# Kernel tuning notes

Measured on AMD Instinct MI355X. Metric: run time of the kernel, lower is better.

Reference implementation:

```python
import jax, jax.numpy as jnp
import numpy as np

N = 50000       # nodes
E = 800000      # edges (avg degree 16)
IN_FEATS = 256
HEADS = 8
OUT_FEATS = 32
SLOPE = 0.2     # LeakyReLU negative slope


def setup_inputs() -> dict:
    key = jax.random.key(0)
    k1, k2, k3, k4, k5, k6 = jax.random.split(key, 6)
    feat = jax.random.normal(k1, (N, IN_FEATS), dtype=jnp.float32)
    # xavier-ish scaling for the linear weight, stored [in, out] for jax
    fc_w = jax.random.normal(k2, (IN_FEATS, HEADS * OUT_FEATS), dtype=jnp.float32) / np.sqrt(IN_FEATS)
    attn_l = jax.random.normal(k3, (HEADS, OUT_FEATS), dtype=jnp.float32) * 0.1
    attn_r = jax.random.normal(k4, (HEADS, OUT_FEATS), dtype=jnp.float32) * 0.1
    src = jax.random.randint(k5, (E,), 0, N, dtype=jnp.int32)
    dst = jnp.sort(jax.random.randint(k6, (E,), 0, N, dtype=jnp.int32))
    return {"feat": feat, "fc_w": fc_w, "attn_l": attn_l, "attn_r": attn_r,
            "src": src, "dst": dst}


def reference(feat, fc_w, attn_l, attn_r, src, dst):
    # dense projection: [N, H, F]
    feat_src = (feat @ fc_w).reshape(N, HEADS, OUT_FEATS)
    el = jnp.einsum('nhf,hf->nh', feat_src, attn_l)   # [N, H]
    er = jnp.einsum('nhf,hf->nh', feat_src, attn_r)   # [N, H]

    # per-edge raw score: nb.el + v.er  -> [E, H]
    e = el[src] + er[dst]
    # per-destination max over incoming edges (edge softmax stabilizer)
    m = jax.ops.segment_max(e, dst, num_segments=N)   # [N, H]
    z = e - m[dst]
    # Seastar order: exp(leaky_relu(emb - max(embs)))
    coeff = jnp.exp(jnp.where(z >= 0, z, SLOPE * z))  # [E, H]
    s = jax.ops.segment_sum(coeff, dst, num_segments=N)
    alpha = coeff / s[dst]                            # [E, H]

    # weighted scatter-sum of gathered neighbor features -> [N, H, F]
    out = jax.ops.segment_sum(alpha[:, :, None] * feat_src[src], dst, num_segments=N)
    return out
```

## Files before the change

kernel.cpp:

```cpp
#include <hip/hip_runtime.h>
#include <hip/hip_bf16.h>

#define N_NODES 50000
#define N_EDGES 800000
#define IN_F 256
#define HEADS 8
#define OUT_F 32
#define HF (HEADS * OUT_F)
#define SLOPE 0.2f

typedef __attribute__((ext_vector_type(8))) short bf16x8;
typedef __attribute__((ext_vector_type(4))) float f32x4;

__device__ __forceinline__ ushort f2bf(float f) {
  union { float f; unsigned u; } x;
  x.f = f;
  unsigned r = x.u + 0x7FFFu + ((x.u >> 16) & 1u);
  return (ushort)(r >> 16);
}

__device__ __forceinline__ float bf2f_lo(unsigned u) {
  return __uint_as_float(u << 16);
}
__device__ __forceinline__ float bf2f_hi(unsigned u) {
  return __uint_as_float(u & 0xFFFF0000u);
}

__global__ void wt_kernel(const float* __restrict__ fc_w,
                          ushort* __restrict__ Bt) {
  __shared__ float tile[32][33];
  const int bx = blockIdx.x * 32;
  const int by = blockIdx.y * 32;
  const int tx = threadIdx.x;
  const int ty = threadIdx.y;
#pragma unroll
  for (int i = 0; i < 32; i += 8)
    tile[ty + i][tx] = fc_w[(size_t)(by + ty + i) * HF + bx + tx];
  __syncthreads();
#pragma unroll
  for (int i = 0; i < 32; i += 8)
    Bt[(size_t)(bx + ty + i) * IN_F + by + tx] = f2bf(tile[tx][ty + i]);
}

#define BM 64
#define BN 256
#define BK 32
#define LDA 40

__global__ __launch_bounds__(256) void gemm_mfma(
    const float* __restrict__ A, const ushort* __restrict__ Bt,
    ushort* __restrict__ Cb, int M) {
  __shared__ __align__(16) ushort As[BM * LDA];
  __shared__ __align__(16) ushort Bs[BN * LDA];

  const int t = threadIdx.x;
  const int wave = t >> 6;
  const int lane = t & 63;
  const int m0 = blockIdx.x * BM;

  const int ar = t >> 2;
  const int ak = (t & 3) * 8;
  const int br = t >> 2;
  const int bk = (t & 3) * 8;

  const int q = lane >> 4;
  const int l16 = lane & 15;
  const int wn = wave * 64;

  f32x4 acc[4][4] = {};

  for (int k0 = 0; k0 < IN_F; k0 += BK) {
    {
      float4 v0 = make_float4(0.f, 0.f, 0.f, 0.f);
      float4 v1 = make_float4(0.f, 0.f, 0.f, 0.f);
      if (m0 + ar < M) {
        const float* ap = &A[(size_t)(m0 + ar) * IN_F + k0 + ak];
        v0 = *(const float4*)ap;
        v1 = *(const float4*)(ap + 4);
      }
      union { ushort s[8]; uint4 v; } u;
      u.s[0] = f2bf(v0.x); u.s[1] = f2bf(v0.y);
      u.s[2] = f2bf(v0.z); u.s[3] = f2bf(v0.w);
      u.s[4] = f2bf(v1.x); u.s[5] = f2bf(v1.y);
      u.s[6] = f2bf(v1.z); u.s[7] = f2bf(v1.w);
      *(uint4*)&As[ar * LDA + ak] = u.v;
    }
#pragma unroll
    for (int i = 0; i < 4; ++i) {
      const int n = br + i * 64;
      *(uint4*)&Bs[n * LDA + bk] =
          *(const uint4*)&Bt[(size_t)n * IN_F + k0 + bk];
    }
    __syncthreads();

    bf16x8 aF[4], bF[4];
#pragma unroll
    for (int i = 0; i < 4; ++i)
      aF[i] = *(const bf16x8*)&As[(i * 16 + l16) * LDA + q * 8];
#pragma unroll
    for (int jj = 0; jj < 4; ++jj)
      bF[jj] = *(const bf16x8*)&Bs[(wn + jj * 16 + l16) * LDA + q * 8];
#pragma unroll
    for (int i = 0; i < 4; ++i)
#pragma unroll
      for (int jj = 0; jj < 4; ++jj)
        acc[i][jj] = __builtin_amdgcn_mfma_f32_16x16x32_bf16(
            aF[i], bF[jj], acc[i][jj], 0, 0, 0);
    __syncthreads();
  }

#pragma unroll
  for (int i = 0; i < 4; ++i) {
#pragma unroll
    for (int r = 0; r < 4; ++r) {
      const int row = m0 + 16 * i + q * 4 + r;
      if (row < M) {
#pragma unroll
        for (int jj = 0; jj < 4; ++jj) {
          const int col = wn + 16 * jj + l16;
          Cb[(size_t)row * HF + col] = f2bf(acc[i][jj][r]);
        }
      }
    }
  }
}

__global__ void wl_kernel(const float* __restrict__ fc_w,
                          const float* __restrict__ attn_l,
                          float* __restrict__ wl) {
  const int idx = blockIdx.x * blockDim.x + threadIdx.x;
  const int k = idx >> 3;
  const int h = idx & 7;
  const float* fp = &fc_w[(size_t)k * HF + h * OUT_F];
  const float* ap = &attn_l[h * OUT_F];
  float acc = 0.f;
#pragma unroll
  for (int f = 0; f < OUT_F; f += 4) {
    float4 a = *(const float4*)&fp[f];
    float4 b = *(const float4*)&ap[f];
    acc += a.x * b.x + a.y * b.y + a.z * b.z + a.w * b.w;
  }
  wl[idx] = acc;
}

__global__ __launch_bounds__(256) void el_kernel(
    const float* __restrict__ feat, const float* __restrict__ wl,
    float* __restrict__ el, int NH) {
  __shared__ float wls[IN_F * HEADS];
  const int t = threadIdx.x;
#pragma unroll
  for (int i = 0; i < (IN_F * HEADS) / 256; ++i)
    wls[i * 256 + t] = wl[i * 256 + t];
  __syncthreads();

  const int idx = blockIdx.x * 256 + t;
  if (idx >= NH) return;
  const int n = idx >> 3;
  const int h = idx & 7;
  const float* fp = &feat[(size_t)n * IN_F];
  float acc = 0.f;
#pragma unroll 8
  for (int k0 = 0; k0 < IN_F; k0 += 4) {
    float4 v = *(const float4*)&fp[k0];
    acc += v.x * wls[(k0 + 0) * 8 + h] + v.y * wls[(k0 + 1) * 8 + h] +
           v.z * wls[(k0 + 2) * 8 + h] + v.w * wls[(k0 + 3) * 8 + h];
  }
  el[idx] = acc;
}

__global__ void rowptr_kernel(const int* __restrict__ dst,
                              int* __restrict__ row_ptr, int N, int E) {
  int i = blockIdx.x * blockDim.x + threadIdx.x;
  if (i > N) return;
  int lo = 0, hi = E;
  while (lo < hi) {
    int mid = (lo + hi) >> 1;
    if (dst[mid] < i) lo = mid + 1; else hi = mid;
  }
  row_ptr[i] = lo;
}

#define CHUNK 64

__global__ __launch_bounds__(256) void aggregate_kernel(
    const ushort* __restrict__ featb, const float* __restrict__ el,
    const int* __restrict__ src, const int* __restrict__ row_ptr,
    float* __restrict__ out) {
  const int v = blockIdx.x;
  const int t = threadIdx.x;
  const int beg = row_ptr[v];
  const int deg = row_ptr[v + 1] - beg;

  if (deg == 0) {
    out[(size_t)v * HF + t] = 0.f;
    return;
  }

  __shared__ float s_wred[4][HEADS];
  __shared__ __align__(16) float s_alpha[CHUNK][HEADS];
  __shared__ int s_src[CHUNK];
  __shared__ __align__(16) float s_out[4][HF];

  const int lane = t & 63;
  const int wave = t >> 6;
  const int j = t >> 3;
  const int h8 = t & 7;
  const int h = lane >> 3;

  float mx = -1e30f;
  for (int e = j; e < deg; e += 32)
    mx = fmaxf(mx, el[(size_t)src[beg + e] * HEADS + h8]);
  mx = fmaxf(mx, __shfl_xor(mx, 8));
  mx = fmaxf(mx, __shfl_xor(mx, 16));
  mx = fmaxf(mx, __shfl_xor(mx, 32));
  if (lane < HEADS) s_wred[wave][lane] = mx;
  __syncthreads();
  const float m = fmaxf(fmaxf(s_wred[0][h8], s_wred[1][h8]),
                        fmaxf(s_wred[2][h8], s_wred[3][h8]));

  float4 acc = make_float4(0.f, 0.f, 0.f, 0.f);
  float ssum = 0.f;

  for (int c0 = 0; c0 < deg; c0 += CHUNK) {
    const int cn = min(CHUNK, deg - c0);
    const int cnp = (cn + 3) & ~3;
    __syncthreads();
    for (int cc = j; cc < cnp; cc += 32) {
      if (cc < cn) {
        const int s = src[beg + c0 + cc];
        if (h8 == 0) s_src[cc] = s;
        const float z = el[(size_t)s * HEADS + h8] - m;
        const float w = (z >= 0.f) ? z : SLOPE * z;
        const float cf = __expf(w);
        s_alpha[cc][h8] = cf;
        ssum += cf;
      } else {
        if (h8 == 0) s_src[cc] = 0;
        s_alpha[cc][h8] = 0.f;
      }
    }
    __syncthreads();
#pragma unroll 2
    for (int e0 = 0; e0 < cnp; e0 += 4) {
      const int e = e0 + wave;
      const int s = s_src[e];
      const float a = s_alpha[e][h];
      const uint2 u = *(const uint2*)&featb[(size_t)s * HF + lane * 4];
      acc.x = fmaf(a, bf2f_lo(u.x), acc.x);
      acc.y = fmaf(a, bf2f_hi(u.x), acc.y);
      acc.z = fmaf(a, bf2f_lo(u.y), acc.z);
      acc.w = fmaf(a, bf2f_hi(u.y), acc.w);
    }
  }

  ssum += __shfl_xor(ssum, 8);
  ssum += __shfl_xor(ssum, 16);
  ssum += __shfl_xor(ssum, 32);
  if (lane < HEADS) s_wred[wave][lane] = ssum;
  *(float4*)&s_out[wave][lane * 4] = acc;
  __syncthreads();

  const int ho = t >> 5;
  const float ssum_all =
      s_wred[0][ho] + s_wred[1][ho] + s_wred[2][ho] + s_wred[3][ho];
  const float r = s_out[0][t] + s_out[1][t] + s_out[2][t] + s_out[3][t];
  out[(size_t)v * HF + t] = r / ssum_all;
}

extern "C" void kernel_launch(void* const* d_in, const int* in_sizes, int n_in,
                              void* d_out, int out_size, void* d_ws,
                              size_t ws_size, hipStream_t stream) {
  const float* feat = (const float*)d_in[0];
  const float* fc_w = (const float*)d_in[1];
  const float* attn_l = (const float*)d_in[2];
  const int* src = (const int*)d_in[4];
  const int* dst = (const int*)d_in[5];
  float* out = (float*)d_out;

  const int N = N_NODES;
  const int E = N_EDGES;

  ushort* featb = (ushort*)d_ws;
  float* el = (float*)(featb + (size_t)N * HF);
  float* wl = el + (size_t)N * HEADS;
  ushort* Bt = (ushort*)(wl + IN_F * HEADS);
  int* row_ptr = (int*)(Bt + (size_t)IN_F * HF);

  wt_kernel<<<dim3(8, 8), dim3(32, 8), 0, stream>>>(fc_w, Bt);

  gemm_mfma<<<(N + BM - 1) / BM, 256, 0, stream>>>(feat, Bt, featb, N);

  wl_kernel<<<(IN_F * HEADS) / 256, 256, 0, stream>>>(fc_w, attn_l, wl);

  el_kernel<<<(N * HEADS + 255) / 256, 256, 0, stream>>>(feat, wl, el,
                                                         N * HEADS);

  rowptr_kernel<<<(N + 1 + 255) / 256, 256, 0, stream>>>(dst, row_ptr, N, E);

  aggregate_kernel<<<N, 256, 0, stream>>>(featb, el, src, row_ptr, out);
}
```

Before: 250.0 us.

## Merge prep kernels, transpose wl in LDS, prefetch neighbor features for low-degree nodes

Three small setup kernels (weight transpose, wl projection, row_ptr binary search) become one launch with block-index dispatch, cutting launch overhead. el_kernel stores wl transposed per head in LDS so each thread can read float4 weights instead of strided scalars. For nodes with degree up to 64, aggregate_kernel issues all neighbor feature gathers into registers before the max/softmax phase, so gather latency overlaps with the score computation and one chunk sync is removed. The prefetch uses 16 uint2 registers per thread, which raises register pressure and may lower occupancy.

After: 264.3 us. 1.06x slower.

```diff
diff --git a/kernel.cpp b/kernel.cpp
--- a/kernel.cpp
+++ b/kernel.cpp
@@ -26,20 +26,56 @@
   return __uint_as_float(u & 0xFFFF0000u);
 }
 
-__global__ void wt_kernel(const float* __restrict__ fc_w,
-                          ushort* __restrict__ Bt) {
+#define ROWPTR_BLOCKS ((N_NODES + 1 + 255) / 256)
+
+__global__ __launch_bounds__(256) void prep_kernel(
+    const float* __restrict__ fc_w, const float* __restrict__ attn_l,
+    ushort* __restrict__ Bt, float* __restrict__ wl,
+    const int* __restrict__ dst, int* __restrict__ row_ptr) {
   __shared__ float tile[32][33];
-  const int bx = blockIdx.x * 32;
-  const int by = blockIdx.y * 32;
-  const int tx = threadIdx.x;
-  const int ty = threadIdx.y;
-#pragma unroll
-  for (int i = 0; i < 32; i += 8)
-    tile[ty + i][tx] = fc_w[(size_t)(by + ty + i) * HF + bx + tx];
-  __syncthreads();
-#pragma unroll
-  for (int i = 0; i < 32; i += 8)
-    Bt[(size_t)(bx + ty + i) * IN_F + by + tx] = f2bf(tile[tx][ty + i]);
+  const int b = blockIdx.x;
+  const int t = threadIdx.x;
+
+  if (b < 64) {
+    const int bx = (b & 7) * 32;
+    const int by = (b >> 3) * 32;
+    const int tx = t & 31;
+    const int ty = t >> 5;
+#pragma unroll
+    for (int i = 0; i < 32; i += 8)
+      tile[ty + i][tx] = fc_w[(size_t)(by + ty + i) * HF + bx + tx];
+    __syncthreads();
+#pragma unroll
+    for (int i = 0; i < 32; i += 8)
+      Bt[(size_t)(bx + ty + i) * IN_F + by + tx] = f2bf(tile[tx][ty + i]);
+  } else if (b == 64) {
+#pragma unroll
+    for (int ii = 0; ii < 8; ++ii) {
+      const int idx = ii * 256 + t;
+      const int k = idx >> 3;
+      const int h = idx & 7;
+      const float* fp = &fc_w[(size_t)k * HF + h * OUT_F];
+      const float* ap = &attn_l[h * OUT_F];
+      float acc = 0.f;
+#pragma unroll
+      for (int f = 0; f < OUT_F; f += 4) {
+        float4 a = *(const float4*)&fp[f];
+        float4 bb = *(const float4*)&ap[f];
+        acc += a.x * bb.x + a.y * bb.y + a.z * bb.z + a.w * bb.w;
+      }
+      wl[idx] = acc;
+    }
+  } else {
+    const int i = (b - 65) * 256 + t;
+    if (i <= N_NODES) {
+      int lo = 0, hi = N_EDGES;
+      while (lo < hi) {
+        int mid = (lo + hi) >> 1;
+        if (dst[mid] < i) lo = mid + 1; else hi = mid;
+      }
+      row_ptr[i] = lo;
+    }
+  }
 }
 
 #define BM 64
@@ -125,32 +161,16 @@
   }
 }
 
-__global__ void wl_kernel(const float* __restrict__ fc_w,
-                          const float* __restrict__ attn_l,
-                          float* __restrict__ wl) {
-  const int idx = blockIdx.x * blockDim.x + threadIdx.x;
-  const int k = idx >> 3;
-  const int h = idx & 7;
-  const float* fp = &fc_w[(size_t)k * HF + h * OUT_F];
-  const float* ap = &attn_l[h * OUT_F];
-  float acc = 0.f;
-#pragma unroll
-  for (int f = 0; f < OUT_F; f += 4) {
-    float4 a = *(const float4*)&fp[f];
-    float4 b = *(const float4*)&ap[f];
-    acc += a.x * b.x + a.y * b.y + a.z * b.z + a.w * b.w;
-  }
-  wl[idx] = acc;
-}
-
 __global__ __launch_bounds__(256) void el_kernel(
     const float* __restrict__ feat, const float* __restrict__ wl,
     float* __restrict__ el, int NH) {
-  __shared__ float wls[IN_F * HEADS];
+  __shared__ __align__(16) float wlsT[HEADS][IN_F + 4];
   const int t = threadIdx.x;
 #pragma unroll
-  for (int i = 0; i < (IN_F * HEADS) / 256; ++i)
-    wls[i * 256 + t] = wl[i * 256 + t];
+  for (int i = 0; i < (IN_F * HEADS) / 256; ++i) {
+    const int idx = i * 256 + t;
+    wlsT[idx & 7][idx >> 3] = wl[idx];
+  }
   __syncthreads();
 
   const int idx = blockIdx.x * 256 + t;
@@ -158,29 +178,16 @@
   const int n = idx >> 3;
   const int h = idx & 7;
   const float* fp = &feat[(size_t)n * IN_F];
+  const float* wp = &wlsT[h][0];
   float acc = 0.f;
 #pragma unroll 8
   for (int k0 = 0; k0 < IN_F; k0 += 4) {
     float4 v = *(const float4*)&fp[k0];
-    acc += v.x * wls[(k0 + 0) * 8 + h] + v.y * wls[(k0 + 1) * 8 + h] +
-           v.z * wls[(k0 + 2) * 8 + h] + v.w * wls[(k0 + 3) * 8 + h];
+    float4 w = *(const float4*)&wp[k0];
+    acc += v.x * w.x + v.y * w.y + v.z * w.z + v.w * w.w;
   }
   el[idx] = acc;
 }
-
-__global__ void rowptr_kernel(const int* __restrict__ dst,
-                              int* __restrict__ row_ptr, int N, int E) {
-  int i = blockIdx.x * blockDim.x + threadIdx.x;
-  if (i > N) return;
-  int lo = 0, hi = E;
-  while (lo < hi) {
-    int mid = (lo + hi) >> 1;
-    if (dst[mid] < i) lo = mid + 1; else hi = mid;
-  }
-  row_ptr[i] = lo;
-}
-
-#define CHUNK 64
 
 __global__ __launch_bounds__(256) void aggregate_kernel(
     const ushort* __restrict__ featb, const float* __restrict__ el,
@@ -196,9 +203,9 @@
     return;
   }
 
-  __shared__ float s_wred[4][HEADS];
-  __shared__ __align__(16) float s_alpha[CHUNK][HEADS];
-  __shared__ int s_src[CHUNK];
+  __shared__ float s_wred[8][HEADS];
+  __shared__ __align__(16) float s_alpha[64][HEADS];
+  __shared__ int s_src[64];
   __shared__ __align__(16) float s_out[4][HF];
 
   const int lane = t & 63;
@@ -207,62 +214,116 @@
   const int h8 = t & 7;
   const int h = lane >> 3;
 
-  float mx = -1e30f;
-  for (int e = j; e < deg; e += 32)
-    mx = fmaxf(mx, el[(size_t)src[beg + e] * HEADS + h8]);
-  mx = fmaxf(mx, __shfl_xor(mx, 8));
-  mx = fmaxf(mx, __shfl_xor(mx, 16));
-  mx = fmaxf(mx, __shfl_xor(mx, 32));
-  if (lane < HEADS) s_wred[wave][lane] = mx;
-  __syncthreads();
-  const float m = fmaxf(fmaxf(s_wred[0][h8], s_wred[1][h8]),
-                        fmaxf(s_wred[2][h8], s_wred[3][h8]));
-
   float4 acc = make_float4(0.f, 0.f, 0.f, 0.f);
   float ssum = 0.f;
 
-  for (int c0 = 0; c0 < deg; c0 += CHUNK) {
-    const int cn = min(CHUNK, deg - c0);
-    const int cnp = (cn + 3) & ~3;
-    __syncthreads();
-    for (int cc = j; cc < cnp; cc += 32) {
-      if (cc < cn) {
-        const int s = src[beg + c0 + cc];
-        if (h8 == 0) s_src[cc] = s;
-        const float z = el[(size_t)s * HEADS + h8] - m;
-        const float w = (z >= 0.f) ? z : SLOPE * z;
-        const float cf = __expf(w);
-        s_alpha[cc][h8] = cf;
-        ssum += cf;
-      } else {
-        if (h8 == 0) s_src[cc] = 0;
-        s_alpha[cc][h8] = 0.f;
-      }
-    }
-    __syncthreads();
+  if (deg <= 64) {
+    const int nIter = (deg > wave) ? ((deg - wave + 3) >> 2) : 0;
+    uint2 q[16];
+#pragma unroll
+    for (int i = 0; i < 16; ++i) {
+      if (i < nIter) {
+        const int s = src[beg + wave + 4 * i];
+        q[i] = *(const uint2*)&featb[(size_t)s * HF + lane * 4];
+      }
+    }
+    float v1 = 0.f, v2 = 0.f;
+    float mx = -1e30f;
+    if (j < deg) {
+      v1 = el[(size_t)src[beg + j] * HEADS + h8];
+      mx = v1;
+    }
+    if (j + 32 < deg) {
+      v2 = el[(size_t)src[beg + j + 32] * HEADS + h8];
+      mx = fmaxf(mx, v2);
+    }
+    mx = fmaxf(mx, __shfl_xor(mx, 8));
+    mx = fmaxf(mx, __shfl_xor(mx, 16));
+    mx = fmaxf(mx, __shfl_xor(mx, 32));
+    if (lane < HEADS) s_wred[wave][lane] = mx;
+    __syncthreads();
+    const float m = fmaxf(fmaxf(s_wred[0][h8], s_wred[1][h8]),
+                          fmaxf(s_wred[2][h8], s_wred[3][h8]));
+    if (j < deg) {
+      const float z = v1 - m;
+      const float w = (z >= 0.f) ? z : SLOPE * z;
+      const float cf = __expf(w);
+      s_alpha[j][h8] = cf;
+      ssum += cf;
+    }
+    if (j + 32 < deg) {
+      const float z = v2 - m;
+      const float w = (z >= 0.f) ? z : SLOPE * z;
+      const float cf = __expf(w);
+      s_alpha[j + 32][h8] = cf;
+      ssum += cf;
+    }
+    __syncthreads();
+#pragma unroll
+    for (int i = 0; i < 16; ++i) {
+      if (i < nIter) {
+        const float a = s_alpha[wave + 4 * i][h];
+        acc.x = fmaf(a, bf2f_lo(q[i].x), acc.x);
+        acc.y = fmaf(a, bf2f_hi(q[i].x), acc.y);
+        acc.z = fmaf(a, bf2f_lo(q[i].y), acc.z);
+        acc.w = fmaf(a, bf2f_hi(q[i].y), acc.w);
+      }
+    }
+  } else {
+    float mx = -1e30f;
+    for (int e = j; e < deg; e += 32)
+      mx = fmaxf(mx, el[(size_t)src[beg + e] * HEADS + h8]);
+    mx = fmaxf(mx, __shfl_xor(mx, 8));
+    mx = fmaxf(mx, __shfl_xor(mx, 16));
+    mx = fmaxf(mx, __shfl_xor(mx, 32));
+    if (lane < HEADS) s_wred[wave][lane] = mx;
+    __syncthreads();
+    const float m = fmaxf(fmaxf(s_wred[0][h8], s_wred[1][h8]),
+                          fmaxf(s_wred[2][h8], s_wred[3][h8]));
+
+    for (int c0 = 0; c0 < deg; c0 += 64) {
+      const int cn = min(64, deg - c0);
+      const int cnp = (cn + 3) & ~3;
+      __syncthreads();
+      for (int cc = j; cc < cnp; cc += 32) {
+        if (cc < cn) {
+          const int s = src[beg + c0 + cc];
+          if (h8 == 0) s_src[cc] = s;
+          const float z = el[(size_t)s * HEADS + h8] - m;
+          const float w = (z >= 0.f) ? z : SLOPE * z;
+          const float cf = __expf(w);
+          s_alpha[cc][h8] = cf;
+          ssum += cf;
+        } else {
+          if (h8 == 0) s_src[cc] = 0;
+          s_alpha[cc][h8] = 0.f;
+        }
+      }
+      __syncthreads();
 #pragma unroll 2
-    for (int e0 = 0; e0 < cnp; e0 += 4) {
-      const int e = e0 + wave;
-      const int s = s_src[e];
-      const float a = s_alpha[e][h];
-      const uint2 u = *(const uint2*)&featb[(size_t)s * HF + lane * 4];
-      acc.x = fmaf(a, bf2f_lo(u.x), acc.x);
-      acc.y = fmaf(a, bf2f_hi(u.x), acc.y);
-      acc.z = fmaf(a, bf2f_lo(u.y), acc.z);
-      acc.w = fmaf(a, bf2f_hi(u.y), acc.w);
+      for (int e0 = 0; e0 < cnp; e0 += 4) {
+        const int e = e0 + wave;
+        const int s = s_src[e];
+        const float a = s_alpha[e][h];
+        const uint2 u = *(const uint2*)&featb[(size_t)s * HF + lane * 4];
+        acc.x = fmaf(a, bf2f_lo(u.x), acc.x);
+        acc.y = fmaf(a, bf2f_hi(u.x), acc.y);
+        acc.z = fmaf(a, bf2f_lo(u.y), acc.z);
+        acc.w = fmaf(a, bf2f_hi(u.y), acc.w);
+      }
     }
   }
 
   ssum += __shfl_xor(ssum, 8);
   ssum += __shfl_xor(ssum, 16);
   ssum += __shfl_xor(ssum, 32);
-  if (lane < HEADS) s_wred[wave][lane] = ssum;
+  if (lane < HEADS) s_wred[4 + wave][lane] = ssum;
   *(float4*)&s_out[wave][lane * 4] = acc;
   __syncthreads();
 
   const int ho = t >> 5;
   const float ssum_all =
-      s_wred[0][ho] + s_wred[1][ho] + s_wred[2][ho] + s_wred[3][ho];
+      s_wred[4][ho] + s_wred[5][ho] + s_wred[6][ho] + s_wred[7][ho];
   const float r = s_out[0][t] + s_out[1][t] + s_out[2][t] + s_out[3][t];
   out[(size_t)v * HF + t] = r / ssum_all;
 }
@@ -278,7 +339,6 @@
   float* out = (float*)d_out;
 
   const int N = N_NODES;
-  const int E = N_EDGES;
 
   ushort* featb = (ushort*)d_ws;
   float* el = (float*)(featb + (size_t)N * HF);
@@ -286,16 +346,13 @@
   ushort* Bt = (ushort*)(wl + IN_F * HEADS);
   int* row_ptr = (int*)(Bt + (size_t)IN_F * HF);
 
-  wt_kernel<<<dim3(8, 8), dim3(32, 8), 0, stream>>>(fc_w, Bt);
+  prep_kernel<<<65 + ROWPTR_BLOCKS, 256, 0, stream>>>(fc_w, attn_l, Bt, wl,
+                                                      dst, row_ptr);
 
   gemm_mfma<<<(N + BM - 1) / BM, 256, 0, stream>>>(feat, Bt, featb, N);
-
-  wl_kernel<<<(IN_F * HEADS) / 256, 256, 0, stream>>>(fc_w, attn_l, wl);
 
   el_kernel<<<(N * HEADS + 255) / 256, 256, 0, stream>>>(feat, wl, el,
                                                          N * HEADS);
 
-  rowptr_kernel<<<(N + 1 + 255) / 256, 256, 0, stream>>>(dst, row_ptr, N, E);
-
   aggregate_kernel<<<N, 256, 0, stream>>>(featb, el, src, row_ptr, out);
 }
```
